# Optimization experiments

Measured on AMD Instinct MI355X. Metric: run time of the kernel, lower is better.

Reference implementation:

```python
import jax, jax.numpy as jnp
import numpy as np
from functools import partial

L, H, D, T_MAX = 12, 12, 768, 256
HD = D // H
FULL = 302  # 100+100+30+72
LN_EPS = 1e-5


def _ln(x, g, b):
    m = jnp.mean(x, axis=-1, keepdims=True)
    v = jnp.mean((x - m) ** 2, axis=-1, keepdims=True)
    return (x - m) * jax.lax.rsqrt(v + LN_EPS) * g + b


def setup_inputs() -> dict:
    key = jax.random.key(0)
    ks = iter(jax.random.split(key, 40))
    B, T = 64, 256
    w = lambda *s: jax.random.normal(next(ks), s, dtype=jnp.float32) * 0.02
    inp = {
        'idxs': jax.random.randint(next(ks), (B, T, 4), 0, 30, dtype=jnp.int32),
        'lat_emb': w(100, 192), 'lon_emb': w(100, 192),
        'sog_emb': w(30, 192), 'cog_emb': w(72, 192),
        'pos_emb': jnp.zeros((1, T_MAX, D), jnp.float32),
        'ln1_g': jnp.ones((L, D)), 'ln1_b': jnp.zeros((L, D)),
        'ln2_g': jnp.ones((L, D)), 'ln2_b': jnp.zeros((L, D)),
        'Wq': w(L, D, D), 'bq': jnp.zeros((L, D)),
        'Wk': w(L, D, D), 'bk': jnp.zeros((L, D)),
        'Wv': w(L, D, D), 'bv': jnp.zeros((L, D)),
        'Wo': w(L, D, D), 'bo': jnp.zeros((L, D)),
        'W1': w(L, D, 4 * D), 'b1': jnp.zeros((L, 4 * D)),
        'W2': w(L, 4 * D, D), 'b2': jnp.zeros((L, D)),
        'lnf_g': jnp.ones((D,)), 'lnf_b': jnp.zeros((D,)),
        'Whead': w(D, FULL),
    }
    return inp


def _transformer(idxs, lat_emb, lon_emb, sog_emb, cog_emb, pos_emb,
                 ln1_g, ln1_b, ln2_g, ln2_b, Wq, bq, Wk, bk, Wv, bv, Wo, bo,
                 W1, b1, W2, b2, lnf_g, lnf_b, Whead):
    B, T, _ = idxs.shape
    # four-hot embedding: concat of the four attribute embeddings -> [B,T,768]
    h = jnp.concatenate([
        lat_emb[idxs[..., 0]], lon_emb[idxs[..., 1]],
        sog_emb[idxs[..., 2]], cog_emb[idxs[..., 3]],
    ], axis=-1) + pos_emb[:, :T]
    causal = jnp.tril(jnp.ones((T, T), dtype=bool))  # [T,T]
    scale = 1.0 / np.sqrt(HD)

    def block(h, p):
        (g1, b1_, g2, b2_, wq, bq_, wk, bk_, wv, bv_, wo, bo_,
         w1, bf1, w2, bf2) = p
        x = _ln(h, g1, b1_)
        q = (x @ wq + bq_).reshape(B, T, H, HD)
        k = (x @ wk + bk_).reshape(B, T, H, HD)
        v = (x @ wv + bv_).reshape(B, T, H, HD)
        att = jnp.einsum('bqhd,bkhd->bhqk', q, k) * scale
        att = jnp.where(causal, att, -jnp.inf)
        att = jax.nn.softmax(att, axis=-1)
        y = jnp.einsum('bhqk,bkhd->bqhd', att, v).reshape(B, T, D)
        h = h + y @ wo + bo_
        x = _ln(h, g2, b2_)
        h = h + jax.nn.gelu(x @ w1 + bf1, approximate=False) @ w2 + bf2
        return h, None

    stacked = (ln1_g, ln1_b, ln2_g, ln2_b, Wq, bq, Wk, bk, Wv, bv, Wo, bo,
               W1, b1, W2, b2)
    h, _ = jax.lax.scan(block, h, stacked)
    h = _ln(h, lnf_g, lnf_b)
    return h @ Whead  # [B,T,302] logits


def reference(idxs, lat_emb, lon_emb, sog_emb, cog_emb, pos_emb,
              ln1_g, ln1_b, ln2_g, ln2_b, Wq, bq, Wk, bk, Wv, bv, Wo, bo,
              W1, b1, W2, b2, lnf_g, lnf_b, Whead):
    return _transformer(idxs, lat_emb, lon_emb, sog_emb, cog_emb, pos_emb,
                        ln1_g, ln1_b, ln2_g, ln2_b, Wq, bq, Wk, bk, Wv, bv,
                        Wo, bo, W1, b1, W2, b2, lnf_g, lnf_b, Whead)
```

## Files before the change

kernel.cpp:

```cpp
#include <hip/hip_runtime.h>
#include <math.h>


#define LNUM 12
#define HNUM 12
#define DDIM 768
#define HDIM 64
#define TSEQ 256
#define NTOK 16384
#define DFF  3072
#define QKS  1536
#define NOUTC 302
#define NOUTP 384

typedef unsigned short u16;
typedef __attribute__((ext_vector_type(8))) __bf16 bf16x8;
typedef __attribute__((ext_vector_type(8))) unsigned short u16x8;
typedef __attribute__((ext_vector_type(4))) float f32x4;

__device__ __forceinline__ u16 f2bf(float f) {
    union { float f; unsigned u; } v; v.f = f;
    return (u16)((v.u + 0x7fff + ((v.u >> 16) & 1)) >> 16);
}

__device__ __forceinline__ void gl2lds16(const u16* g, u16* l) {
    __builtin_amdgcn_global_load_lds(
        (const __attribute__((address_space(1))) void*)g,
        (__attribute__((address_space(3))) void*)l, 16, 0, 0);
}

__global__ __launch_bounds__(256)
void embed_kernel(const int* __restrict__ idxs, const float* __restrict__ lat,
                  const float* __restrict__ lon, const float* __restrict__ sog,
                  const float* __restrict__ cog, const float* __restrict__ pos,
                  float* __restrict__ h) {
    int i = blockIdx.x * 256 + threadIdx.x;
    int tok = i / DDIM, d = i - tok * DDIM;
    int t = tok & (TSEQ - 1);
    int tab = d / 192, sub = d - tab * 192;
    const float* tp = (tab == 0) ? lat : (tab == 1) ? lon : (tab == 2) ? sog : cog;
    int row = idxs[tok * 4 + tab];
    h[i] = tp[row * 192 + sub] + pos[t * DDIM + d];
}

__global__ __launch_bounds__(256)
void ln_kernel(const float* __restrict__ in, u16* __restrict__ out,
               const float* __restrict__ g, const float* __restrict__ b) {
    const int row = blockIdx.x, t = threadIdx.x;
    const float* x = in + (size_t)row * DDIM;
    float v0 = x[t], v1 = x[t + 256], v2 = x[t + 512];
    float s = v0 + v1 + v2;
    float sq = v0 * v0 + v1 * v1 + v2 * v2;
    #pragma unroll
    for (int m = 32; m; m >>= 1) { s += __shfl_xor(s, m); sq += __shfl_xor(sq, m); }
    __shared__ float red[8];
    const int w = t >> 6;
    if ((t & 63) == 0) { red[w] = s; red[4 + w] = sq; }
    __syncthreads();
    s  = red[0] + red[1] + red[2] + red[3];
    sq = red[4] + red[5] + red[6] + red[7];
    const float mean = s * (1.f / DDIM);
    const float rstd = rsqrtf(sq * (1.f / DDIM) - mean * mean + 1e-5f);
    u16* o = out + (size_t)row * DDIM;
    o[t]       = f2bf((v0 - mean) * rstd * g[t]       + b[t]);
    o[t + 256] = f2bf((v1 - mean) * rstd * g[t + 256] + b[t + 256]);
    o[t + 512] = f2bf((v2 - mean) * rstd * g[t + 512] + b[t + 512]);
}

__global__ __launch_bounds__(256)
void wconv_kernel(const float* __restrict__ in, u16* __restrict__ out,
                  int R, int C, int Cpad) {
    __shared__ float tile[32][33];
    const float* src = in + (size_t)blockIdx.z * R * C;
    u16* dst = out + (size_t)blockIdx.z * (size_t)Cpad * R;
    const int c0 = blockIdx.x * 32, r0 = blockIdx.y * 32;
    const int tx = threadIdx.x & 31, ty = threadIdx.x >> 5;
    #pragma unroll
    for (int i = 0; i < 4; ++i) {
        int r = r0 + ty + i * 8, c = c0 + tx;
        tile[ty + i * 8][tx] = (c < C) ? src[(size_t)r * C + c] : 0.f;
    }
    __syncthreads();
    #pragma unroll
    for (int i = 0; i < 4; ++i) {
        int oc = c0 + ty + i * 8;
        dst[(size_t)oc * R + r0 + tx] = f2bf(tile[tx][ty + i * 8]);
    }
}


#define LDA8(MQ) \
  _Pragma("unroll") for (int mt = 0; mt < 4; ++mt) { \
    a[mt][0] = __builtin_bit_cast(bf16x8, *(const u16x8*)(A0p + (MQ)*8192 + mt*1024)); \
    a[mt][1] = __builtin_bit_cast(bf16x8, *(const u16x8*)(A1p + (MQ)*8192 + mt*1024)); }

#define LDB4(NQ, BR) \
  _Pragma("unroll") for (int nt = 0; nt < 2; ++nt) { \
    BR[nt][0] = __builtin_bit_cast(bf16x8, *(const u16x8*)(B0p + (NQ)*8192 + nt*1024)); \
    BR[nt][1] = __builtin_bit_cast(bf16x8, *(const u16x8*)(B1p + (NQ)*8192 + nt*1024)); }

#define MMA16(MQ, NQ, BR) \
  __builtin_amdgcn_s_barrier(); \
  asm volatile("s_waitcnt lgkmcnt(0)" ::: "memory"); \
  __builtin_amdgcn_s_setprio(1); \
  _Pragma("unroll") for (int mt = 0; mt < 4; ++mt) \
  _Pragma("unroll") for (int nt = 0; nt < 2; ++nt) { \
    acc[(MQ)*4+mt][(NQ)*2+nt] = __builtin_amdgcn_mfma_f32_16x16x32_bf16(a[mt][0], BR[nt][0], acc[(MQ)*4+mt][(NQ)*2+nt], 0, 0, 0); \
    acc[(MQ)*4+mt][(NQ)*2+nt] = __builtin_amdgcn_mfma_f32_16x16x32_bf16(a[mt][1], BR[nt][1], acc[(MQ)*4+mt][(NQ)*2+nt], 0, 0, 0); } \
  __builtin_amdgcn_s_setprio(0);

#define STGA(NXT, H, KT) { \
  const u16* s_ = gA + (size_t)((H) * 128) * K + (size_t)(KT) * 64; \
  u16* d_ = &Sh[NXT][H][0][0] + w * 512; \
  gl2lds16(s_, d_); gl2lds16(s_ + (size_t)64 * K, d_ + 4096); }

#define STGB(NXT, H, KT) { \
  const u16* s_ = gB + (size_t)((H) * 128) * K + (size_t)(KT) * 64; \
  u16* d_ = &Sh[NXT][2 + (H)][0][0] + w * 512; \
  gl2lds16(s_, d_); gl2lds16(s_ + (size_t)64 * K, d_ + 4096); }

#define VM4 asm volatile("s_waitcnt vmcnt(4)" ::: "memory");
#define VM2 asm volatile("s_waitcnt vmcnt(2)" ::: "memory");
#define VM0 asm volatile("s_waitcnt vmcnt(0)" ::: "memory");
#define VMN

#define KTILE(CUR, KT, STG, VA, VB, VC) { \
  const u16* A0p = aQ0 + (CUR) * 32768; const u16* A1p = aQ1 + (CUR) * 32768; \
  const u16* B0p = bQ0 + (CUR) * 32768; const u16* B1p = bQ1 + (CUR) * 32768; \
   LDA8(0) LDB4(0, b0) if (STG) STGA(1 - (CUR), 0, (KT) + 1) \
         MMA16(0, 0, b0) VA __builtin_amdgcn_s_barrier(); \
   LDB4(1, b1) if (STG) STGB(1 - (CUR), 0, (KT) + 1) \
         MMA16(0, 1, b1) VB __builtin_amdgcn_s_barrier(); \
   LDA8(1) if (STG) STGB(1 - (CUR), 1, (KT) + 1) \
         MMA16(1, 1, b1) __builtin_amdgcn_s_barrier(); \
   if (STG) STGA(1 - (CUR), 1, (KT) + 1) \
         MMA16(1, 0, b0) VC __builtin_amdgcn_s_barrier(); \
}

template <int MODE>
__global__ __launch_bounds__(512, 2)
void gemm256(const u16* __restrict__ A, const u16* __restrict__ Bt,
             const float* __restrict__ bias, const float* __restrict__ bias2,
             const float* __restrict__ bias3, const float* __restrict__ res,
             void* __restrict__ Cout, int M, int N, int K) {
    (void)M;
    __shared__ u16 Sh[2][4][128][64] __attribute__((aligned(16)));
    const int t = threadIdx.x;
    const int w = t >> 6, l = t & 63;
    const int wm = w >> 2, wn = w & 3;
    const int fm = l & 15, fq = l >> 4;
    const int nwg = (int)(gridDim.x * gridDim.y);
    int lin = (int)(blockIdx.y * gridDim.x + blockIdx.x);
    const int cpx = nwg >> 3;
    lin = (lin & 7) * cpx + (lin >> 3);
    const int bm = (lin & 63) * 256, bn = (lin >> 6) * 256;
    const int srow = (w << 3) + (l >> 3);
    const int schunk = (l & 7) ^ ((l >> 3) & 7);
    const u16* gA = A + (size_t)(bm + srow) * K + schunk * 8;
    const u16* gB = Bt + (size_t)(bn + srow) * K + schunk * 8;
    const int aoff0 = fm * 64 + ((fq ^ (fm & 7)) << 3);
    const int aoff1 = aoff0 ^ 32;
    const u16* aQ0 = &Sh[0][0][0][0] + wm * 4096 + aoff0;
    const u16* aQ1 = &Sh[0][0][0][0] + wm * 4096 + aoff1;
    const u16* bQ0 = &Sh[0][2][0][0] + wn * 2048 + aoff0;
    const u16* bQ1 = &Sh[0][2][0][0] + wn * 2048 + aoff1;
    f32x4 acc[8][4];
    #pragma unroll
    for (int i = 0; i < 8; ++i)
        #pragma unroll
        for (int j = 0; j < 4; ++j) acc[i][j] = (f32x4){0.f, 0.f, 0.f, 0.f};
    bf16x8 a[4][2], b0[2][2], b1[2][2];
    STGA(0, 0, 0) STGB(0, 0, 0) STGB(0, 1, 0) STGA(0, 1, 0)
    asm volatile("s_waitcnt vmcnt(4)" ::: "memory");
    __builtin_amdgcn_s_barrier();
    const int nkt = K >> 6;
    for (int kt = 0; kt < nkt - 2; kt += 2) {
        KTILE(0, kt,     true, VM4, VM4, VM4)
        KTILE(1, kt + 1, true, VM4, VM4, VM4)
    }
    KTILE(0, nkt - 2, true,  VM4, VM4, VM4)
    KTILE(1, nkt - 1, false, VM2, VM0, VMN)
    #pragma unroll
    for (int m8 = 0; m8 < 8; ++m8) {
        const int row0 = bm + (m8 >> 2) * 128 + wm * 64 + (m8 & 3) * 16 + fq * 4;
        #pragma unroll
        for (int n4 = 0; n4 < 4; ++n4) {
            const int col = bn + (n4 >> 1) * 128 + wn * 32 + (n4 & 1) * 16 + fm;
            float bv;
            if (MODE == 5) {
                bv = (col < 768) ? bias[col] : (col < 1536) ? bias2[col - 768] : bias3[col - 1536];
            } else {
                bv = bias[col];
            }
            #pragma unroll
            for (int i = 0; i < 4; ++i) {
                const int row = row0 + i;
                float v = acc[m8][n4][i] + bv;
                if (MODE == 1) {
                    v = 0.5f * v * (1.f + erff(v * 0.70710678118654752f));
                    ((u16*)Cout)[(size_t)row * N + col] = f2bf(v);
                } else if (MODE == 2) {
                    ((float*)Cout)[(size_t)row * N + col] = v + res[(size_t)row * N + col];
                } else {
                    if (col < 1536) {
                        ((u16*)Cout)[(size_t)row * QKS + col] = f2bf(v);
                    } else {
                        const int c = col - 1536;
                        const int bb = row >> 8, tt = row & 255;
                        const int hh = c >> 6, dd = c & 63;
                        u16* vt = (u16*)Cout + (size_t)NTOK * QKS;
                        vt[(((size_t)(bb * HNUM + hh)) * HDIM + dd) * TSEQ + tt] = f2bf(v);
                    }
                }
            }
        }
    }
}

template <int MODE>
__global__ __launch_bounds__(256)
void gemm_bt(const u16* __restrict__ A, const u16* __restrict__ Bt,
             const float* __restrict__ bias, const float* __restrict__ bias2,
             const float* __restrict__ bias3, const float* __restrict__ res,
             void* __restrict__ Cout, int M, int N, int K, int ncut) {
    __shared__ u16 As[3][128][32] __attribute__((aligned(16)));
    __shared__ u16 Bs[3][128][32] __attribute__((aligned(16)));
    const int t = threadIdx.x;
    const int w = t >> 6, lane = t & 63;
    const int bm = blockIdx.x * 128, bn = blockIdx.y * 128;
    const int moff = (w >> 1) * 64, noff = (w & 1) * 64;
    const int lrow = t >> 2, lcol = (t & 3) * 8;
    const int fm = lane & 15, fq = lane >> 4;
    const f32x4 zero = {0.f, 0.f, 0.f, 0.f};
    f32x4 acc[4][4];
    #pragma unroll
    for (int a = 0; a < 4; ++a)
        #pragma unroll
        for (int c = 0; c < 4; ++c) acc[a][c] = zero;
    const u16* pA = A + (size_t)(bm + lrow) * K + lcol;
    const u16* pB = Bt + (size_t)(bn + lrow) * K + lcol;
    const size_t rstep = (size_t)64 * K;
    const int wr = w << 4;
    auto stage = [&](int s, int b) {
        const u16* ga = pA + s * 32;
        const u16* gb = pB + s * 32;
        gl2lds16(ga,         &As[b][wr][0]);
        gl2lds16(ga + rstep, &As[b][wr + 64][0]);
        gl2lds16(gb,         &Bs[b][wr][0]);
        gl2lds16(gb + rstep, &Bs[b][wr + 64][0]);
    };
    const int kts = K >> 5;
    stage(0, 0);
    stage(1, 1);
    int bcur = 0, bpre = 2;
    for (int kt = 0; kt < kts; ++kt) {
        if (kt + 2 < kts) stage(kt + 2, bpre);
        const int ahead = kts - 1 - kt;
        if (ahead >= 2)      asm volatile("s_waitcnt vmcnt(8)" ::: "memory");
        else if (ahead == 1) asm volatile("s_waitcnt vmcnt(4)" ::: "memory");
        else                 asm volatile("s_waitcnt vmcnt(0)" ::: "memory");
        __builtin_amdgcn_s_barrier();
        bf16x8 af[4], bfr[4];
        #pragma unroll
        for (int mt = 0; mt < 4; ++mt)
            af[mt] = __builtin_bit_cast(bf16x8, *(const u16x8*)&As[bcur][moff + mt * 16 + fm][fq * 8]);
        #pragma unroll
        for (int nt = 0; nt < 4; ++nt)
            bfr[nt] = __builtin_bit_cast(bf16x8, *(const u16x8*)&Bs[bcur][noff + nt * 16 + fm][fq * 8]);
        asm volatile("s_waitcnt lgkmcnt(0)" ::: "memory");
        __builtin_amdgcn_s_barrier();
        #pragma unroll
        for (int mt = 0; mt < 4; ++mt)
            #pragma unroll
            for (int nt = 0; nt < 4; ++nt)
                acc[mt][nt] = __builtin_amdgcn_mfma_f32_16x16x32_bf16(af[mt], bfr[nt], acc[mt][nt], 0, 0, 0);
        bcur = (bcur == 2) ? 0 : bcur + 1;
        bpre = (bpre == 2) ? 0 : bpre + 1;
    }
    #pragma unroll
    for (int mt = 0; mt < 4; ++mt) {
        #pragma unroll
        for (int nt = 0; nt < 4; ++nt) {
            const int col = bn + noff + nt * 16 + fm;
            float bv = 0.f;
            if (MODE == 5) {
                bv = (col < 768) ? bias[col] : (col < 1536) ? bias2[col - 768] : bias3[col - 1536];
            } else if (MODE != 3) {
                bv = bias[col];
            }
            #pragma unroll
            for (int i = 0; i < 4; ++i) {
                const int row = bm + moff + mt * 16 + fq * 4 + i;
                float v = acc[mt][nt][i] + bv;
                if (MODE == 0) {
                    ((u16*)Cout)[(size_t)row * N + col] = f2bf(v);
                } else if (MODE == 1) {
                    v = 0.5f * v * (1.f + erff(v * 0.70710678118654752f));
                    ((u16*)Cout)[(size_t)row * N + col] = f2bf(v);
                } else if (MODE == 2) {
                    ((float*)Cout)[(size_t)row * N + col] = v + res[(size_t)row * N + col];
                } else if (MODE == 3) {
                    if (col < ncut) ((float*)Cout)[(size_t)row * ncut + col] = v;
                } else {
                    if (col < 1536) {
                        ((u16*)Cout)[(size_t)row * QKS + col] = f2bf(v);
                    } else {
                        const int c = col - 1536;
                        const int bb = row >> 8, tt = row & 255;
                        const int hh = c >> 6, dd = c & 63;
                        u16* vt = (u16*)Cout + (size_t)NTOK * QKS;
                        vt[(((size_t)(bb * HNUM + hh)) * HDIM + dd) * TSEQ + tt] = f2bf(v);
                    }
                }
            }
        }
    }
}

__global__ __launch_bounds__(256)
void attn_kernel(const u16* __restrict__ QK, const u16* __restrict__ Vt,
                 u16* __restrict__ Yb) {
    __shared__ u16 Pt[4][256][16] __attribute__((aligned(16)));
    const int bh = blockIdx.x;
    const int b = bh / HNUM, hh = bh - b * HNUM;
    const int w = threadIdx.x >> 6, lane = threadIdx.x & 63;
    const int fm = lane & 15, fq = lane >> 4;
    const int qt = blockIdx.y * 4 + w;
    const size_t qrow0 = (size_t)b * TSEQ;
    const int col0 = hh * HDIM;
    const u16* qp = QK + (qrow0 + qt * 16 + fm) * QKS + col0 + fq * 8;
    const bf16x8 aq0 = __builtin_bit_cast(bf16x8, *(const u16x8*)qp);
    const bf16x8 aq1 = __builtin_bit_cast(bf16x8, *(const u16x8*)(qp + 32));
    f32x4 s[16];
    #pragma unroll
    for (int kt = 0; kt < 16; ++kt) {
        if (kt <= qt) {
            const u16* kp = QK + (qrow0 + kt * 16 + fm) * QKS + 768 + col0 + fq * 8;
            bf16x8 bk0 = __builtin_bit_cast(bf16x8, *(const u16x8*)kp);
            bf16x8 bk1 = __builtin_bit_cast(bf16x8, *(const u16x8*)(kp + 32));
            f32x4 z = {0.f, 0.f, 0.f, 0.f};
            z = __builtin_amdgcn_mfma_f32_16x16x32_bf16(aq0, bk0, z, 0, 0, 0);
            z = __builtin_amdgcn_mfma_f32_16x16x32_bf16(aq1, bk1, z, 0, 0, 0);
            s[kt] = z;
        }
    }
    float lrow[4];
    #pragma unroll
    for (int i = 0; i < 4; ++i) {
        float mx = -1e30f;
        #pragma unroll
        for (int kt = 0; kt < 16; ++kt) {
            if (kt <= qt) {
                const bool valid = (kt < qt) || (fm <= fq * 4 + i);
                const float v = valid ? s[kt][i] * 0.125f : -1e30f;
                s[kt][i] = v;
                mx = fmaxf(mx, v);
            }
        }
        #pragma unroll
        for (int d = 1; d < 16; d <<= 1) mx = fmaxf(mx, __shfl_xor(mx, d));
        float sum = 0.f;
        #pragma unroll
        for (int kt = 0; kt < 16; ++kt) {
            if (kt <= qt) {
                const float e = __expf(s[kt][i] - mx);
                s[kt][i] = e;
                sum += e;
            }
        }
        #pragma unroll
        for (int d = 1; d < 16; d <<= 1) sum += __shfl_xor(sum, d);
        lrow[i] = sum;
    }
    const int nks = (qt + 2) >> 1;
    #pragma unroll
    for (int kt = 0; kt < 16; ++kt) {
        if (kt < 2 * nks) {
            unsigned lo = 0, hi = 0;
            if (kt <= qt) {
                lo = (unsigned)f2bf(s[kt][0]) | ((unsigned)f2bf(s[kt][1]) << 16);
                hi = (unsigned)f2bf(s[kt][2]) | ((unsigned)f2bf(s[kt][3]) << 16);
            }
            uint2 pk; pk.x = lo; pk.y = hi;
            *(uint2*)&Pt[w][kt * 16 + fm][fq * 4] = pk;
        }
    }
    __syncthreads();
    f32x4 o[4];
    #pragma unroll
    for (int dt = 0; dt < 4; ++dt) o[dt] = (f32x4){0.f, 0.f, 0.f, 0.f};
    #pragma unroll
    for (int ks = 0; ks < 8; ++ks) {
        if (ks < nks) {
            u16x8 praw;
            #pragma unroll
            for (int j = 0; j < 8; ++j) praw[j] = Pt[w][ks * 32 + fq * 8 + j][fm];
            const bf16x8 pa = __builtin_bit_cast(bf16x8, praw);
            #pragma unroll
            for (int dt = 0; dt < 4; ++dt) {
                const u16* vp = Vt + ((size_t)bh * HDIM + dt * 16 + fm) * TSEQ + ks * 32 + fq * 8;
                const bf16x8 bv = __builtin_bit_cast(bf16x8, *(const u16x8*)vp);
                o[dt] = __builtin_amdgcn_mfma_f32_16x16x32_bf16(pa, bv, o[dt], 0, 0, 0);
            }
        }
    }
    #pragma unroll
    for (int i = 0; i < 4; ++i) {
        const float inv = 1.f / lrow[i];
        #pragma unroll
        for (int dt = 0; dt < 4; ++dt)
            Yb[(qrow0 + qt * 16 + fq * 4 + i) * DDIM + col0 + dt * 16 + fm] = f2bf(o[dt][i] * inv);
    }
}

extern "C" void kernel_launch(void* const* d_in, const int* in_sizes, int n_in,
                              void* d_out, int out_size, void* d_ws, size_t ws_size,
                              hipStream_t stream) {
    (void)in_sizes; (void)n_in; (void)out_size; (void)ws_size;
    const int*   idxs  = (const int*)d_in[0];
    const float* lat   = (const float*)d_in[1];
    const float* lon   = (const float*)d_in[2];
    const float* sog   = (const float*)d_in[3];
    const float* cog   = (const float*)d_in[4];
    const float* pos   = (const float*)d_in[5];
    const float* ln1_g = (const float*)d_in[6];
    const float* ln1_b = (const float*)d_in[7];
    const float* ln2_g = (const float*)d_in[8];
    const float* ln2_b = (const float*)d_in[9];
    const float* Wq = (const float*)d_in[10];
    const float* bq = (const float*)d_in[11];
    const float* Wk = (const float*)d_in[12];
    const float* bk = (const float*)d_in[13];
    const float* Wv = (const float*)d_in[14];
    const float* bv = (const float*)d_in[15];
    const float* Wo = (const float*)d_in[16];
    const float* bo = (const float*)d_in[17];
    const float* W1 = (const float*)d_in[18];
    const float* b1 = (const float*)d_in[19];
    const float* W2 = (const float*)d_in[20];
    const float* b2 = (const float*)d_in[21];
    const float* lnf_g = (const float*)d_in[22];
    const float* lnf_b = (const float*)d_in[23];
    const float* Whead = (const float*)d_in[24];

    char* base = (char*)d_ws;
    size_t off = 0;
    auto carve = [&](size_t bytes) { void* r = base + off; off += (bytes + 255) & ~(size_t)255; return r; };
    float* h  = (float*)carve((size_t)NTOK * DDIM * 4);
    u16* xb = (u16*)carve((size_t)NTOK * DDIM * 2);
    u16* qk = (u16*)carve((size_t)NTOK * QKS * 2);
    u16* vt = (u16*)carve((size_t)NTOK * DDIM * 2);
    u16* yb = (u16*)carve((size_t)NTOK * DDIM * 2);
    u16* ub = qk;
    u16* WtQKV = (u16*)carve((size_t)3 * DDIM * DDIM * 2);
    u16* WtO = (u16*)carve((size_t)DDIM * DDIM * 2);
    u16* Wt1 = (u16*)carve((size_t)DDIM * DFF * 2);
    u16* Wt2 = (u16*)carve((size_t)DFF * DDIM * 2);
    u16* WtH = (u16*)carve((size_t)NOUTP * DDIM * 2);

    embed_kernel<<<NTOK * DDIM / 256, 256, 0, stream>>>(idxs, lat, lon, sog, cog, pos, h);

    const dim3 G768(64, 3), G3072(64, 12), GQKV(64, 9), ghead(128, 3);
    const dim3 tq(24, 24, 1), t1(96, 24, 1), t2(24, 96, 1);
    const size_t wsq = (size_t)DDIM * DDIM, wsf = (size_t)DDIM * DFF;
    for (int l = 0; l < LNUM; ++l) {
        wconv_kernel<<<tq, 256, 0, stream>>>(Wq + l * wsq, WtQKV, DDIM, DDIM, DDIM);
        wconv_kernel<<<tq, 256, 0, stream>>>(Wk + l * wsq, WtQKV + wsq, DDIM, DDIM, DDIM);
        wconv_kernel<<<tq, 256, 0, stream>>>(Wv + l * wsq, WtQKV + 2 * wsq, DDIM, DDIM, DDIM);
        wconv_kernel<<<tq, 256, 0, stream>>>(Wo + l * wsq, WtO, DDIM, DDIM, DDIM);
        wconv_kernel<<<t1, 256, 0, stream>>>(W1 + l * wsf, Wt1, DDIM, DFF, DFF);
        wconv_kernel<<<t2, 256, 0, stream>>>(W2 + l * wsf, Wt2, DFF, DDIM, DDIM);

        ln_kernel<<<NTOK, 256, 0, stream>>>(h, xb, ln1_g + l * DDIM, ln1_b + l * DDIM);
        gemm256<5><<<GQKV, 512, 0, stream>>>(xb, WtQKV, bq + l * DDIM, bk + l * DDIM,
                                             bv + l * DDIM, nullptr, qk,
                                             NTOK, 3 * DDIM, DDIM);
        attn_kernel<<<dim3(768, 4), 256, 0, stream>>>(qk, vt, yb);
        gemm256<2><<<G768, 512, 0, stream>>>(yb, WtO, bo + l * DDIM, nullptr, nullptr, h, h,
                                             NTOK, DDIM, DDIM);
        ln_kernel<<<NTOK, 256, 0, stream>>>(h, xb, ln2_g + l * DDIM, ln2_b + l * DDIM);
        gemm256<1><<<G3072, 512, 0, stream>>>(xb, Wt1, b1 + l * DFF, nullptr, nullptr, nullptr, ub,
                                              NTOK, DFF, DDIM);
        gemm256<2><<<G768, 512, 0, stream>>>(ub, Wt2, b2 + l * DDIM, nullptr, nullptr, h, h,
                                             NTOK, DDIM, DFF);
    }
    ln_kernel<<<NTOK, 256, 0, stream>>>(h, xb, lnf_g, lnf_b);
    wconv_kernel<<<dim3(NOUTP / 32, DDIM / 32, 1), 256, 0, stream>>>(Whead, WtH, DDIM, NOUTC, NOUTP);
    gemm_bt<3><<<ghead, 256, 0, stream>>>(xb, WtH, nullptr, nullptr, nullptr, nullptr, d_out,
                                          NTOK, NOUTP, DDIM, NOUTC);
}
```

Baseline: 6.789 ms.

## Split-K the FFN down-projection with atomics and triple-buffer A tiles in GEMM

The W2 GEMM (K=3072) is split four ways along K on a 3D grid, giving 768 workgroups instead of 192. Each split adds its partial into the fp32 residual stream with atomic adds, and only the first split adds the bias. The shared GEMM kernel now triple-buffers A tiles, prefetching two k-steps ahead, while B stays double-buffered. This is meant to improve occupancy and latency hiding, at the cost of atomic traffic, a non-deterministic summation order, and more LDS per block, which may limit two blocks per CU. Dead modes were also dropped from gemm_bt.

```diff
diff --git a/kernel.cpp b/kernel.cpp
--- a/kernel.cpp
+++ b/kernel.cpp
@@ -109,32 +109,37 @@
     acc[(MQ)*4+mt][(NQ)*2+nt] = __builtin_amdgcn_mfma_f32_16x16x32_bf16(a[mt][1], BR[nt][1], acc[(MQ)*4+mt][(NQ)*2+nt], 0, 0, 0); } \
   __builtin_amdgcn_s_setprio(0);
 
-#define STGA(NXT, H, KT) { \
+#define STGAH(DST, H, KT) { \
   const u16* s_ = gA + (size_t)((H) * 128) * K + (size_t)(KT) * 64; \
-  u16* d_ = &Sh[NXT][H][0][0] + w * 512; \
+  u16* d_ = (DST) + (H) * 8192 + w * 512; \
   gl2lds16(s_, d_); gl2lds16(s_ + (size_t)64 * K, d_ + 4096); }
 
-#define STGB(NXT, H, KT) { \
+#define STGBH(DST, H, KT) { \
   const u16* s_ = gB + (size_t)((H) * 128) * K + (size_t)(KT) * 64; \
-  u16* d_ = &Sh[NXT][2 + (H)][0][0] + w * 512; \
+  u16* d_ = (DST) + (H) * 8192 + w * 512; \
   gl2lds16(s_, d_); gl2lds16(s_ + (size_t)64 * K, d_ + 4096); }
 
 #define VM4 asm volatile("s_waitcnt vmcnt(4)" ::: "memory");
 #define VM2 asm volatile("s_waitcnt vmcnt(2)" ::: "memory");
 #define VM0 asm volatile("s_waitcnt vmcnt(0)" ::: "memory");
 #define VMN
-
-#define KTILE(CUR, KT, STG, VA, VB, VC) { \
-  const u16* A0p = aQ0 + (CUR) * 32768; const u16* A1p = aQ1 + (CUR) * 32768; \
-  const u16* B0p = bQ0 + (CUR) * 32768; const u16* B1p = bQ1 + (CUR) * 32768; \
-   LDA8(0) LDB4(0, b0) if (STG) STGA(1 - (CUR), 0, (KT) + 1) \
-         MMA16(0, 0, b0) VA __builtin_amdgcn_s_barrier(); \
-   LDB4(1, b1) if (STG) STGB(1 - (CUR), 0, (KT) + 1) \
-         MMA16(0, 1, b1) VB __builtin_amdgcn_s_barrier(); \
-   LDA8(1) if (STG) STGB(1 - (CUR), 1, (KT) + 1) \
-         MMA16(1, 1, b1) __builtin_amdgcn_s_barrier(); \
-   if (STG) STGA(1 - (CUR), 1, (KT) + 1) \
-         MMA16(1, 0, b0) VC __builtin_amdgcn_s_barrier(); \
+#define BARR __builtin_amdgcn_s_barrier();
+
+#define KTILE_S(VW1, VW4, SGA, SGB, KT) { \
+  const u16* A0p = Acur + wmoff + aoff0; \
+  const u16* A1p = Acur + wmoff + aoff1; \
+  const u16* B0p = Bcur + wnoff + aoff0; \
+  const u16* B1p = Bcur + wnoff + aoff1; \
+   LDA8(0) LDB4(0, b0) if (SGA) { STGAH(Astg, 0, (KT) + 2) } \
+         MMA16(0, 0, b0) VW1 BARR \
+   LDB4(1, b1) if (SGB) { STGBH(Bstg, 0, (KT) + 1) } \
+         MMA16(0, 1, b1) BARR \
+   LDA8(1) if (SGB) { STGBH(Bstg, 1, (KT) + 1) } \
+         MMA16(1, 1, b1) BARR \
+   if (SGA) { STGAH(Astg, 1, (KT) + 2) } \
+         MMA16(1, 0, b0) VW4 BARR \
+  u16* tA_ = Acur; Acur = Anxt; Anxt = Astg; Astg = tA_; \
+  u16* tB_ = Bcur; Bcur = Bstg; Bstg = tB_; \
 }
 
 template <int MODE>
@@ -142,44 +147,53 @@
 void gemm256(const u16* __restrict__ A, const u16* __restrict__ Bt,
              const float* __restrict__ bias, const float* __restrict__ bias2,
              const float* __restrict__ bias3, const float* __restrict__ res,
-             void* __restrict__ Cout, int M, int N, int K) {
-    (void)M;
-    __shared__ u16 Sh[2][4][128][64] __attribute__((aligned(16)));
+             void* __restrict__ Cout, int N, int K, int KLOC) {
+    __shared__ u16 Ash[3][2][128][64] __attribute__((aligned(16)));
+    __shared__ u16 Bsh[2][2][128][64] __attribute__((aligned(16)));
     const int t = threadIdx.x;
     const int w = t >> 6, l = t & 63;
     const int wm = w >> 2, wn = w & 3;
     const int fm = l & 15, fq = l >> 4;
-    const int nwg = (int)(gridDim.x * gridDim.y);
-    int lin = (int)(blockIdx.y * gridDim.x + blockIdx.x);
+    const int nwg = (int)(gridDim.x * gridDim.y * gridDim.z);
+    int lin = (int)((blockIdx.z * gridDim.y + blockIdx.y) * gridDim.x + blockIdx.x);
     const int cpx = nwg >> 3;
     lin = (lin & 7) * cpx + (lin >> 3);
-    const int bm = (lin & 63) * 256, bn = (lin >> 6) * 256;
+    const int bm = (lin & 63) * 256;
+    const int rest = lin >> 6;
+    const int bn = (rest % (int)gridDim.y) * 256;
+    const int bz = rest / (int)gridDim.y;
+    const int k0 = bz * KLOC;
     const int srow = (w << 3) + (l >> 3);
     const int schunk = (l & 7) ^ ((l >> 3) & 7);
-    const u16* gA = A + (size_t)(bm + srow) * K + schunk * 8;
-    const u16* gB = Bt + (size_t)(bn + srow) * K + schunk * 8;
+    const u16* gA = A + (size_t)(bm + srow) * K + k0 + schunk * 8;
+    const u16* gB = Bt + (size_t)(bn + srow) * K + k0 + schunk * 8;
     const int aoff0 = fm * 64 + ((fq ^ (fm & 7)) << 3);
     const int aoff1 = aoff0 ^ 32;
-    const u16* aQ0 = &Sh[0][0][0][0] + wm * 4096 + aoff0;
-    const u16* aQ1 = &Sh[0][0][0][0] + wm * 4096 + aoff1;
-    const u16* bQ0 = &Sh[0][2][0][0] + wn * 2048 + aoff0;
-    const u16* bQ1 = &Sh[0][2][0][0] + wn * 2048 + aoff1;
+    const int wmoff = wm * 4096, wnoff = wn * 2048;
+    u16* Acur = &Ash[0][0][0][0];
+    u16* Anxt = &Ash[1][0][0][0];
+    u16* Astg = &Ash[2][0][0][0];
+    u16* Bcur = &Bsh[0][0][0][0];
+    u16* Bstg = &Bsh[1][0][0][0];
     f32x4 acc[8][4];
     #pragma unroll
     for (int i = 0; i < 8; ++i)
         #pragma unroll
         for (int j = 0; j < 4; ++j) acc[i][j] = (f32x4){0.f, 0.f, 0.f, 0.f};
     bf16x8 a[4][2], b0[2][2], b1[2][2];
-    STGA(0, 0, 0) STGB(0, 0, 0) STGB(0, 1, 0) STGA(0, 1, 0)
-    asm volatile("s_waitcnt vmcnt(4)" ::: "memory");
-    __builtin_amdgcn_s_barrier();
-    const int nkt = K >> 6;
-    for (int kt = 0; kt < nkt - 2; kt += 2) {
-        KTILE(0, kt,     true, VM4, VM4, VM4)
-        KTILE(1, kt + 1, true, VM4, VM4, VM4)
-    }
-    KTILE(0, nkt - 2, true,  VM4, VM4, VM4)
-    KTILE(1, nkt - 1, false, VM2, VM0, VMN)
+    STGAH(Acur, 0, 0) STGAH(Acur, 1, 0)
+    STGBH(Bcur, 0, 0) STGBH(Bcur, 1, 0)
+    STGAH(Anxt, 0, 1) STGAH(Anxt, 1, 1)
+    VM4
+    BARR
+    const int nloc = KLOC >> 6;
+    int kt = 0;
+    for (; kt <= nloc - 3; ++kt) {
+        KTILE_S(VM4, VM4, true, true, kt)
+    }
+    KTILE_S(VM2, VM2, false, true, kt)
+    ++kt;
+    KTILE_S(VM0, VMN, false, false, kt)
     #pragma unroll
     for (int m8 = 0; m8 < 8; ++m8) {
         const int row0 = bm + (m8 >> 2) * 128 + wm * 64 + (m8 & 3) * 16 + fq * 4;
@@ -201,6 +215,9 @@
                     ((u16*)Cout)[(size_t)row * N + col] = f2bf(v);
                 } else if (MODE == 2) {
                     ((float*)Cout)[(size_t)row * N + col] = v + res[(size_t)row * N + col];
+                } else if (MODE == 6) {
+                    float av = acc[m8][n4][i] + (bz == 0 ? bv : 0.f);
+                    unsafeAtomicAdd((float*)Cout + (size_t)row * N + col, av);
                 } else {
                     if (col < 1536) {
                         ((u16*)Cout)[(size_t)row * QKS + col] = f2bf(v);
@@ -229,7 +246,7 @@
     const int w = t >> 6, lane = t & 63;
     const int bm = blockIdx.x * 128, bn = blockIdx.y * 128;
     const int moff = (w >> 1) * 64, noff = (w & 1) * 64;
-    const int lrow = t >> 2, lcol = (t & 3) * 8;
+    const int lrow = t >> 2;
     const int fm = lane & 15, fq = lane >> 4;
     const f32x4 zero = {0.f, 0.f, 0.f, 0.f};
     f32x4 acc[4][4];
@@ -237,8 +254,8 @@
     for (int a = 0; a < 4; ++a)
         #pragma unroll
         for (int c = 0; c < 4; ++c) acc[a][c] = zero;
-    const u16* pA = A + (size_t)(bm + lrow) * K + lcol;
-    const u16* pB = Bt + (size_t)(bn + lrow) * K + lcol;
+    const u16* pA = A + (size_t)(bm + lrow) * K + (t & 3) * 8;
+    const u16* pB = Bt + (size_t)(bn + lrow) * K + (t & 3) * 8;
     const size_t rstep = (size_t)64 * K;
     const int wr = w << 4;
     auto stage = [&](int s, int b) {
@@ -283,34 +300,17 @@
         for (int nt = 0; nt < 4; ++nt) {
             const int col = bn + noff + nt * 16 + fm;
             float bv = 0.f;
-            if (MODE == 5) {
-                bv = (col < 768) ? bias[col] : (col < 1536) ? bias2[col - 768] : bias3[col - 1536];
-            } else if (MODE != 3) {
-                bv = bias[col];
-            }
+            if (MODE != 3) bv = bias[col];
             #pragma unroll
             for (int i = 0; i < 4; ++i) {
                 const int row = bm + moff + mt * 16 + fq * 4 + i;
                 float v = acc[mt][nt][i] + bv;
                 if (MODE == 0) {
                     ((u16*)Cout)[(size_t)row * N + col] = f2bf(v);
-                } else if (MODE == 1) {
-                    v = 0.5f * v * (1.f + erff(v * 0.70710678118654752f));
-                    ((u16*)Cout)[(size_t)row * N + col] = f2bf(v);
                 } else if (MODE == 2) {
                     ((float*)Cout)[(size_t)row * N + col] = v + res[(size_t)row * N + col];
                 } else if (MODE == 3) {
                     if (col < ncut) ((float*)Cout)[(size_t)row * ncut + col] = v;
-                } else {
-                    if (col < 1536) {
-                        ((u16*)Cout)[(size_t)row * QKS + col] = f2bf(v);
-                    } else {
-                        const int c = col - 1536;
-                        const int bb = row >> 8, tt = row & 255;
-                        const int hh = c >> 6, dd = c & 63;
-                        u16* vt = (u16*)Cout + (size_t)NTOK * QKS;
-                        vt[(((size_t)(bb * HNUM + hh)) * HDIM + dd) * TSEQ + tt] = f2bf(v);
-                    }
                 }
             }
         }
@@ -460,7 +460,7 @@
 
     embed_kernel<<<NTOK * DDIM / 256, 256, 0, stream>>>(idxs, lat, lon, sog, cog, pos, h);
 
-    const dim3 G768(64, 3), G3072(64, 12), GQKV(64, 9), ghead(128, 3);
+    const dim3 G768(64, 3, 1), G3072(64, 12, 1), GQKV(64, 9, 1), GW2(64, 3, 4), ghead(128, 3);
     const dim3 tq(24, 24, 1), t1(96, 24, 1), t2(24, 96, 1);
     const size_t wsq = (size_t)DDIM * DDIM, wsf = (size_t)DDIM * DFF;
     for (int l = 0; l < LNUM; ++l) {
@@ -474,15 +474,15 @@
         ln_kernel<<<NTOK, 256, 0, stream>>>(h, xb, ln1_g + l * DDIM, ln1_b + l * DDIM);
         gemm256<5><<<GQKV, 512, 0, stream>>>(xb, WtQKV, bq + l * DDIM, bk + l * DDIM,
                                              bv + l * DDIM, nullptr, qk,
-                                             NTOK, 3 * DDIM, DDIM);
+                                             3 * DDIM, DDIM, DDIM);
         attn_kernel<<<dim3(768, 4), 256, 0, stream>>>(qk, vt, yb);
         gemm256<2><<<G768, 512, 0, stream>>>(yb, WtO, bo + l * DDIM, nullptr, nullptr, h, h,
-                                             NTOK, DDIM, DDIM);
+                                             DDIM, DDIM, DDIM);
         ln_kernel<<<NTOK, 256, 0, stream>>>(h, xb, ln2_g + l * DDIM, ln2_b + l * DDIM);
         gemm256<1><<<G3072, 512, 0, stream>>>(xb, Wt1, b1 + l * DFF, nullptr, nullptr, nullptr, ub,
-                                              NTOK, DFF, DDIM);
-        gemm256<2><<<G768, 512, 0, stream>>>(ub, Wt2, b2 + l * DDIM, nullptr, nullptr, h, h,
-                                             NTOK, DDIM, DFF);
+                                              DFF, DDIM, DDIM);
+        gemm256<6><<<GW2, 512, 0, stream>>>(ub, Wt2, b2 + l * DDIM, nullptr, nullptr, nullptr, h,
+                                            DDIM, DFF, DFF / 4);
     }
     ln_kernel<<<NTOK, 256, 0, stream>>>(h, xb, lnf_g, lnf_b);
     wconv_kernel<<<dim3(NOUTP / 32, DDIM / 32, 1), 256, 0, stream>>>(Whead, WtH, DDIM, NOUTC, NOUTP);
```

Result: slower. 8.882 ms (+30.8%).
